# Kernel tuning notes

Measured on AMD Instinct MI355X. Metric: run time of the kernel, lower is better.

Reference implementation:

```python
import jax, jax.numpy as jnp
import numpy as np

B, N, D_IN, D = 4, 256, 128, 256
T = 3
EPS = 1e-5


def _layernorm(x, g, b):
    mu = x.mean(axis=-1, keepdims=True)
    var = x.var(axis=-1, keepdims=True)
    return (x - mu) * jax.lax.rsqrt(var + EPS) * g + b


def setup_inputs() -> dict:
    key = jax.random.key(0)
    ks = jax.random.split(key, 16)
    s = lambda k, shape, fan_in: jax.random.normal(k, shape, jnp.float32) / np.sqrt(fan_in)
    return {
        "inputs": jax.random.normal(ks[0], (B, N, D_IN), jnp.float32),
        "v_t": jax.random.normal(ks[1], (B, N, D), jnp.float32),
        "i_t": jnp.zeros((B, N, N), jnp.float32),
        # proj_inputs
        "Wp": s(ks[2], (D_IN, D), D_IN), "bp": jnp.zeros((D,), jnp.float32),
        # MLPAdjacency
        "Wx": s(ks[3], (D, D), D), "bx": jnp.zeros((D,), jnp.float32),
        "wi": s(ks[4], (D,), 1), "bi": jnp.zeros((D,), jnp.float32),
        "ws": s(ks[5], (D,), D), "bs": jnp.zeros((1,), jnp.float32),
        # LayerNorms
        "g_pre": jnp.ones((3 * D,), jnp.float32), "be_pre": jnp.zeros((3 * D,), jnp.float32),
        "g_n": jnp.ones((D,), jnp.float32), "be_n": jnp.zeros((D,), jnp.float32),
        # DeepSet(3D -> D -> D), equivariant layers: h@Wg + mean(h)@Wl + b
        "W1g": s(ks[6], (3 * D, D), 3 * D), "W1l": s(ks[7], (3 * D, D), 3 * D),
        "b1": jnp.zeros((D,), jnp.float32),
        "W2g": s(ks[8], (D, D), D), "W2l": s(ks[9], (D, D), D),
        "b2": jnp.zeros((D,), jnp.float32),
    }


def reference(inputs, v_t, i_t, Wp, bp, Wx, bx, wi, bi, ws, bs,
              g_pre, be_pre, g_n, be_n, W1g, W1l, b1, W2g, W2l, b2):
    x_in = inputs @ Wp + bp  # [b,n,d]
    n_t, inc = v_t, i_t
    preds = []
    for _ in range(T):
        # MLPAdjacency: [b,n,n,d] broadcast sum -> relu -> linear -> sigmoid
        xp = n_t @ Wx + bx
        s = jax.nn.relu(xp[:, None, :, :] + xp[:, :, None, :]
                        + inc[..., None] * wi + bi)
        inc = jax.nn.sigmoid(jnp.einsum('bend,d->ben', s, ws) + bs[0])  # [b,n,n]
        # aggregation
        upd = jnp.einsum('ben,bed->bnd', inc, n_t)
        # DeepSet over normalized concat, residual + LayerNorm
        h = _layernorm(jnp.concatenate([x_in, n_t, upd], axis=-1), g_pre, be_pre)
        m = h.mean(axis=1, keepdims=True)
        h1 = jax.nn.relu(h @ W1g + m @ W1l + b1)
        m1 = h1.mean(axis=1, keepdims=True)
        h2 = h1 @ W2g + m1 @ W2l + b2
        n_t = _layernorm(n_t + h2, g_n, be_n)
        preds.append(inc)
    return (jnp.stack(preds, axis=0), n_t, inc)
```

## Files before the change

kernel.cpp:

```cpp
#include <hip/hip_runtime.h>
#include <cstddef>

#define LN_EPS 1e-5f

__device__ inline float4 ld4(const float* p) { return *reinterpret_cast<const float4*>(p); }
__device__ inline void st4(float* p, float4 v) { *reinterpret_cast<float4*>(p) = v; }

__device__ __forceinline__ void gemm_dev(float* lds, const float* __restrict__ A,
                                         const float* __restrict__ W,
                                         const float* __restrict__ bias,
                                         float* __restrict__ dst,
                                         int K, int chunk, int row0, int col0, int k0) {
  float* At = lds;
  float* Ws = lds + 1088;
  const int tid = threadIdx.x;
  const int tx = tid & 15, ty = tid >> 4;
  float acc[4][4] = {{0.f}};
  const int arow = tid >> 2;
  const int ak4 = (tid & 3) * 4;
  const int wk = tid >> 4;
  const int wc4 = (tid & 15) * 4;
  for (int ks = 0; ks < chunk; ks += 16) {
    float4 av = ld4(&A[(size_t)(row0 + arow) * K + k0 + ks + ak4]);
    float4 wv = ld4(&W[(size_t)(k0 + ks + wk) * 256 + col0 + wc4]);
    __syncthreads();
    At[(ak4 + 0) * 68 + arow] = av.x;
    At[(ak4 + 1) * 68 + arow] = av.y;
    At[(ak4 + 2) * 68 + arow] = av.z;
    At[(ak4 + 3) * 68 + arow] = av.w;
    st4(&Ws[wk * 68 + wc4], wv);
    __syncthreads();
#pragma unroll
    for (int kk = 0; kk < 16; ++kk) {
      float4 a = ld4(&At[kk * 68 + ty * 4]);
      float4 w = ld4(&Ws[kk * 68 + tx * 4]);
      acc[0][0] = fmaf(a.x, w.x, acc[0][0]); acc[0][1] = fmaf(a.x, w.y, acc[0][1]);
      acc[0][2] = fmaf(a.x, w.z, acc[0][2]); acc[0][3] = fmaf(a.x, w.w, acc[0][3]);
      acc[1][0] = fmaf(a.y, w.x, acc[1][0]); acc[1][1] = fmaf(a.y, w.y, acc[1][1]);
      acc[1][2] = fmaf(a.y, w.z, acc[1][2]); acc[1][3] = fmaf(a.y, w.w, acc[1][3]);
      acc[2][0] = fmaf(a.z, w.x, acc[2][0]); acc[2][1] = fmaf(a.z, w.y, acc[2][1]);
      acc[2][2] = fmaf(a.z, w.z, acc[2][2]); acc[2][3] = fmaf(a.z, w.w, acc[2][3]);
      acc[3][0] = fmaf(a.w, w.x, acc[3][0]); acc[3][1] = fmaf(a.w, w.y, acc[3][1]);
      acc[3][2] = fmaf(a.w, w.z, acc[3][2]); acc[3][3] = fmaf(a.w, w.w, acc[3][3]);
    }
  }
  if (bias) {
    float4 b4 = ld4(&bias[col0 + tx * 4]);
#pragma unroll
    for (int i = 0; i < 4; ++i) {
      float4 o;
      o.x = acc[i][0] + b4.x; o.y = acc[i][1] + b4.y;
      o.z = acc[i][2] + b4.z; o.w = acc[i][3] + b4.w;
      st4(&dst[(size_t)(row0 + ty * 4 + i) * 256 + col0 + tx * 4], o);
    }
  } else {
#pragma unroll
    for (int i = 0; i < 4; ++i) {
      float4 o = {acc[i][0], acc[i][1], acc[i][2], acc[i][3]};
      st4(&dst[(size_t)(row0 + ty * 4 + i) * 256 + col0 + tx * 4], o);
    }
  }
}

__device__ __forceinline__ void gemm_h1(float* lds, const float* __restrict__ part,
                                        const float* __restrict__ mt1p,
                                        const float* __restrict__ W,
                                        float* __restrict__ dst,
                                        int gb, int row0, int col0, int k0) {
  float* At = lds;
  float* Ws = lds + 1088;
  float* mt1s = lds + 2176;
  const int tid = threadIdx.x;
  const int tx = tid & 15, ty = tid >> 4;
  if (tid < 64) {
    float s = 0.f;
#pragma unroll
    for (int k2 = 0; k2 < 12; ++k2) s += mt1p[((size_t)(k2 * 4 + gb) << 8) + k0 + tid];
    mt1s[tid] = s;
  }
  float acc[4][4] = {{0.f}};
  const int arow = tid >> 2;
  const int ak4 = (tid & 3) * 4;
  const int wk = tid >> 4;
  const int wc4 = (tid & 15) * 4;
  for (int ks = 0; ks < 64; ks += 16) {
    size_t ao = (size_t)(row0 + arow) * 256 + k0 + ks + ak4;
    float4 p0 = ld4(&part[ao]);
    float4 p1 = ld4(&part[ao + 262144]);
    float4 p2 = ld4(&part[ao + 524288]);
    float4 p3 = ld4(&part[ao + 786432]);
    float4 wv = ld4(&W[(size_t)(k0 + ks + wk) * 256 + col0 + wc4]);
    __syncthreads();
    float4 m = ld4(&mt1s[ks + ak4]);
    float4 av;
    av.x = fmaxf(p0.x + p1.x + p2.x + p3.x + m.x, 0.f);
    av.y = fmaxf(p0.y + p1.y + p2.y + p3.y + m.y, 0.f);
    av.z = fmaxf(p0.z + p1.z + p2.z + p3.z + m.z, 0.f);
    av.w = fmaxf(p0.w + p1.w + p2.w + p3.w + m.w, 0.f);
    At[(ak4 + 0) * 68 + arow] = av.x;
    At[(ak4 + 1) * 68 + arow] = av.y;
    At[(ak4 + 2) * 68 + arow] = av.z;
    At[(ak4 + 3) * 68 + arow] = av.w;
    st4(&Ws[wk * 68 + wc4], wv);
    __syncthreads();
#pragma unroll
    for (int kk = 0; kk < 16; ++kk) {
      float4 a = ld4(&At[kk * 68 + ty * 4]);
      float4 w = ld4(&Ws[kk * 68 + tx * 4]);
      acc[0][0] = fmaf(a.x, w.x, acc[0][0]); acc[0][1] = fmaf(a.x, w.y, acc[0][1]);
      acc[0][2] = fmaf(a.x, w.z, acc[0][2]); acc[0][3] = fmaf(a.x, w.w, acc[0][3]);
      acc[1][0] = fmaf(a.y, w.x, acc[1][0]); acc[1][1] = fmaf(a.y, w.y, acc[1][1]);
      acc[1][2] = fmaf(a.y, w.z, acc[1][2]); acc[1][3] = fmaf(a.y, w.w, acc[1][3]);
      acc[2][0] = fmaf(a.z, w.x, acc[2][0]); acc[2][1] = fmaf(a.z, w.y, acc[2][1]);
      acc[2][2] = fmaf(a.z, w.z, acc[2][2]); acc[2][3] = fmaf(a.z, w.w, acc[2][3]);
      acc[3][0] = fmaf(a.w, w.x, acc[3][0]); acc[3][1] = fmaf(a.w, w.y, acc[3][1]);
      acc[3][2] = fmaf(a.w, w.z, acc[3][2]); acc[3][3] = fmaf(a.w, w.w, acc[3][3]);
    }
  }
#pragma unroll
  for (int i = 0; i < 4; ++i) {
    float4 o = {acc[i][0], acc[i][1], acc[i][2], acc[i][3]};
    st4(&dst[(size_t)(row0 + ty * 4 + i) * 256 + col0 + tx * 4], o);
  }
}

__device__ __forceinline__ void gemmt_dev(float* lds, const float* __restrict__ pred,
                                          const float* __restrict__ nt,
                                          float* __restrict__ pp,
                                          int gb, int n0, int col0, int k0) {
  float* At = lds;
  float* Ws = lds + 1088;
  const int tid = threadIdx.x;
  const int tx = tid & 15, ty = tid >> 4;
  const float* Ab = pred + ((size_t)gb << 16);
  const float* Bb = nt + ((size_t)gb << 16);
  float acc[4][4] = {{0.f}};
  const int ee = tid >> 4;
  const int q4 = (tid & 15) * 4;
  for (int ks = 0; ks < 64; ks += 16) {
    float4 av = ld4(&Ab[((size_t)(k0 + ks + ee) << 8) + n0 + q4]);
    float4 wv = ld4(&Bb[((size_t)(k0 + ks + ee) << 8) + col0 + q4]);
    __syncthreads();
    st4(&At[ee * 68 + q4], av);
    st4(&Ws[ee * 68 + q4], wv);
    __syncthreads();
#pragma unroll
    for (int kk = 0; kk < 16; ++kk) {
      float4 a = ld4(&At[kk * 68 + ty * 4]);
      float4 w = ld4(&Ws[kk * 68 + tx * 4]);
      acc[0][0] = fmaf(a.x, w.x, acc[0][0]); acc[0][1] = fmaf(a.x, w.y, acc[0][1]);
      acc[0][2] = fmaf(a.x, w.z, acc[0][2]); acc[0][3] = fmaf(a.x, w.w, acc[0][3]);
      acc[1][0] = fmaf(a.y, w.x, acc[1][0]); acc[1][1] = fmaf(a.y, w.y, acc[1][1]);
      acc[1][2] = fmaf(a.y, w.z, acc[1][2]); acc[1][3] = fmaf(a.y, w.w, acc[1][3]);
      acc[2][0] = fmaf(a.z, w.x, acc[2][0]); acc[2][1] = fmaf(a.z, w.y, acc[2][1]);
      acc[2][2] = fmaf(a.z, w.z, acc[2][2]); acc[2][3] = fmaf(a.z, w.w, acc[2][3]);
      acc[3][0] = fmaf(a.w, w.x, acc[3][0]); acc[3][1] = fmaf(a.w, w.y, acc[3][1]);
      acc[3][2] = fmaf(a.w, w.z, acc[3][2]); acc[3][3] = fmaf(a.w, w.w, acc[3][3]);
    }
  }
#pragma unroll
  for (int i = 0; i < 4; ++i) {
    float4 o = {acc[i][0], acc[i][1], acc[i][2], acc[i][3]};
    st4(&pp[(((size_t)gb << 8) + n0 + ty * 4 + i) * 256 + col0 + tx * 4], o);
  }
}

__device__ __forceinline__ void wred2(float& s, float& q) {
#pragma unroll
  for (int off = 32; off; off >>= 1) {
    s += __shfl_xor(s, off);
    q += __shfl_xor(q, off);
  }
}

__device__ __forceinline__ void mtk_dev(float* lds, const float* __restrict__ X,
                                        const float* __restrict__ Wl,
                                        const float* __restrict__ bias,
                                        float* __restrict__ mtp, int gb, int ks, int Kd) {
  float* sm = lds;
  float* m64 = lds + 256;
  const int tid = threadIdx.x;
  const int col = tid & 63, q = tid >> 6;
  const float* xb = X + (size_t)(gb * 256 + q * 64) * Kd + ks * 64 + col;
  float s = 0.f;
#pragma unroll 8
  for (int r = 0; r < 64; ++r) s += xb[(size_t)r * Kd];
  sm[tid] = s;
  __syncthreads();
  if (tid < 64) m64[tid] = (sm[tid] + sm[tid + 64] + sm[tid + 128] + sm[tid + 192]) * (1.f / 256.f);
  __syncthreads();
  const int c = tid;
  float acc = (ks == 0) ? bias[c] : 0.f;
  const float* wp = Wl + (size_t)ks * 64 * 256 + c;
#pragma unroll 8
  for (int k = 0; k < 64; ++k) acc = fmaf(m64[k], wp[(size_t)k * 256], acc);
  mtp[((size_t)(ks * 4 + gb) << 8) + c] = acc;
}

__device__ __forceinline__ void mtk_h1(float* lds, const float* __restrict__ part,
                                       const float* __restrict__ mt1p,
                                       const float* __restrict__ Wl,
                                       const float* __restrict__ bias,
                                       float* __restrict__ mtp, int gb, int ks) {
  float* sm = lds;
  float* m64 = lds + 256;
  const int tid = threadIdx.x;
  const int col = tid & 63, q = tid >> 6;
  float mt1v = 0.f;
#pragma unroll
  for (int k2 = 0; k2 < 12; ++k2) mt1v += mt1p[((size_t)(k2 * 4 + gb) << 8) + ks * 64 + col];
  const float* pb = part + (size_t)(gb * 256 + q * 64) * 256 + ks * 64 + col;
  float s = 0.f;
#pragma unroll 4
  for (int r = 0; r < 64; ++r) {
    size_t o = (size_t)r * 256;
    float v = pb[o] + pb[o + 262144] + pb[o + 524288] + pb[o + 786432] + mt1v;
    s += fmaxf(v, 0.f);
  }
  sm[tid] = s;
  __syncthreads();
  if (tid < 64) m64[tid] = (sm[tid] + sm[tid + 64] + sm[tid + 128] + sm[tid + 192]) * (1.f / 256.f);
  __syncthreads();
  const int c = tid;
  float acc = (ks == 0) ? bias[c] : 0.f;
  const float* wp = Wl + (size_t)ks * 64 * 256 + c;
#pragma unroll 8
  for (int k = 0; k < 64; ++k) acc = fmaf(m64[k], wp[(size_t)k * 256], acc);
  mtp[((size_t)(ks * 4 + gb) << 8) + c] = acc;
}


__global__ __launch_bounds__(256) void k_gemm(const float* __restrict__ A,
                                              const float* __restrict__ W,
                                              const float* __restrict__ bias,
                                              float* __restrict__ dst,
                                              int K, int chunk) {
  __shared__ float lds[2176];
  float* base = bias ? dst : dst + (size_t)blockIdx.z * 262144;
  gemm_dev(lds, A, W, bias, base, K, chunk,
           blockIdx.x * 64, blockIdx.y * 64, blockIdx.z * chunk);
}

__global__ __launch_bounds__(256) void k_adj(const float* __restrict__ part,
                                             const float* __restrict__ incold,
                                             const float* __restrict__ wi,
                                             const float* __restrict__ bi,
                                             const float* __restrict__ bx,
                                             const float* __restrict__ wsv,
                                             const float* __restrict__ bs,
                                             float* __restrict__ pred,
                                             float* __restrict__ pred2) {
  __shared__ float lds[8448];
  float* tn = lds;
  float* te = lds + 32 * 132;
  const int n0 = blockIdx.x * 32, e0 = blockIdx.y * 32, gb = blockIdx.z;
  const int tid = threadIdx.x;
  const size_t rb = (size_t)gb * 256;
  const int tx = tid & 15, ty = tid >> 4;
  float incv[2][2], acc[2][2];
#pragma unroll
  for (int j = 0; j < 2; ++j)
#pragma unroll
    for (int i = 0; i < 2; ++i) {
      incv[j][i] = incold[((rb + e0 + ty + 16 * j) << 8) + n0 + tx + 16 * i];
      acc[j][i] = 0.f;
    }
  for (int dh = 0; dh < 256; dh += 128) {
    if (dh) __syncthreads();
#pragma unroll
    for (int s = 0; s < 4; ++s) {
      int idx = tid + s * 256;
      int row = idx >> 5;
      int d = dh + (idx & 31) * 4;
      float4 bxv = ld4(&bx[d]);
      {
        size_t o = ((rb + n0 + row) << 8) + d;
        float4 p0 = ld4(&part[o]);
        float4 p1 = ld4(&part[o + 262144]);
        float4 p2 = ld4(&part[o + 524288]);
        float4 p3 = ld4(&part[o + 786432]);
        float4 v;
        v.x = p0.x + p1.x + p2.x + p3.x + bxv.x;
        v.y = p0.y + p1.y + p2.y + p3.y + bxv.y;
        v.z = p0.z + p1.z + p2.z + p3.z + bxv.z;
        v.w = p0.w + p1.w + p2.w + p3.w + bxv.w;
        st4(&tn[row * 132 + (d - dh)], v);
      }
      {
        size_t o = ((rb + e0 + row) << 8) + d;
        float4 p0 = ld4(&part[o]);
        float4 p1 = ld4(&part[o + 262144]);
        float4 p2 = ld4(&part[o + 524288]);
        float4 p3 = ld4(&part[o + 786432]);
        float4 bv = ld4(&bi[d]);
        float4 v;
        v.x = p0.x + p1.x + p2.x + p3.x + bxv.x + bv.x;
        v.y = p0.y + p1.y + p2.y + p3.y + bxv.y + bv.y;
        v.z = p0.z + p1.z + p2.z + p3.z + bxv.z + bv.z;
        v.w = p0.w + p1.w + p2.w + p3.w + bxv.w + bv.w;
        st4(&te[row * 132 + (d - dh)], v);
      }
    }
    __syncthreads();
#pragma unroll 4
    for (int dl = 0; dl < 128; dl += 4) {
      float4 wiq = ld4(&wi[dh + dl]);
      float4 wsq = ld4(&wsv[dh + dl]);
      float4 xn0 = ld4(&tn[tx * 132 + dl]);
      float4 xn1 = ld4(&tn[(tx + 16) * 132 + dl]);
      float4 xe0 = ld4(&te[ty * 132 + dl]);
      float4 xe1 = ld4(&te[(ty + 16) * 132 + dl]);
#pragma unroll
      for (int j = 0; j < 2; ++j) {
        float4 xe = j ? xe1 : xe0;
#pragma unroll
        for (int i = 0; i < 2; ++i) {
          float4 xn = i ? xn1 : xn0;
          float u;
          u = fmaf(incv[j][i], wiq.x, xn.x + xe.x); u = fmaxf(u, 0.f); acc[j][i] = fmaf(u, wsq.x, acc[j][i]);
          u = fmaf(incv[j][i], wiq.y, xn.y + xe.y); u = fmaxf(u, 0.f); acc[j][i] = fmaf(u, wsq.y, acc[j][i]);
          u = fmaf(incv[j][i], wiq.z, xn.z + xe.z); u = fmaxf(u, 0.f); acc[j][i] = fmaf(u, wsq.z, acc[j][i]);
          u = fmaf(incv[j][i], wiq.w, xn.w + xe.w); u = fmaxf(u, 0.f); acc[j][i] = fmaf(u, wsq.w, acc[j][i]);
        }
      }
    }
  }
  const float b0 = bs[0];
#pragma unroll
  for (int j = 0; j < 2; ++j)
#pragma unroll
    for (int i = 0; i < 2; ++i) {
      float s = acc[j][i] + b0;
      float v = 1.f / (1.f + __expf(-s));
      size_t o = ((rb + e0 + ty + 16 * j) << 8) + n0 + tx + 16 * i;
      pred[o] = v;
      if (pred2) pred2[o] = v;
    }
}

__global__ __launch_bounds__(256) void k_gemmt(const float* __restrict__ pred,
                                               const float* __restrict__ nt,
                                               float* __restrict__ part) {
  __shared__ float lds[2176];
  const int gb = blockIdx.z >> 2, kc = blockIdx.z & 3;
  gemmt_dev(lds, pred, nt, part + (size_t)kc * 262144,
            gb, blockIdx.x * 64, blockIdx.y * 64, kc * 64);
}

__global__ __launch_bounds__(256) void k_ln768(const float* __restrict__ part,
                                               const float* __restrict__ x_in,
                                               const float* __restrict__ nt,
                                               const float* __restrict__ g,
                                               const float* __restrict__ be,
                                               float* __restrict__ h) {
  const int row = blockIdx.x * 4 + (threadIdx.x >> 6);
  const int lane = threadIdx.x & 63;
  const int c4 = lane * 4;
  const size_t ro = (size_t)row * 256 + c4;
  float4 u = ld4(&part[ro]);
  float4 u1 = ld4(&part[ro + 262144]);
  float4 u2 = ld4(&part[ro + 524288]);
  float4 u3 = ld4(&part[ro + 786432]);
  u.x += u1.x + u2.x + u3.x;
  u.y += u1.y + u2.y + u3.y;
  u.z += u1.z + u2.z + u3.z;
  u.w += u1.w + u2.w + u3.w;
  float4 xi = ld4(&x_in[ro]);
  float4 nv = ld4(&nt[ro]);
  float s = xi.x + xi.y + xi.z + xi.w + nv.x + nv.y + nv.z + nv.w + u.x + u.y + u.z + u.w;
  float sq = xi.x * xi.x + xi.y * xi.y + xi.z * xi.z + xi.w * xi.w
           + nv.x * nv.x + nv.y * nv.y + nv.z * nv.z + nv.w * nv.w
           + u.x * u.x + u.y * u.y + u.z * u.z + u.w * u.w;
  wred2(s, sq);
  float mu = s * (1.f / 768.f);
  float rs = rsqrtf(sq * (1.f / 768.f) - mu * mu + LN_EPS);
  float* hr = h + (size_t)row * 768;
  {
    float4 g4 = ld4(&g[c4]), b4 = ld4(&be[c4]), o;
    o.x = (xi.x - mu) * rs * g4.x + b4.x;
    o.y = (xi.y - mu) * rs * g4.y + b4.y;
    o.z = (xi.z - mu) * rs * g4.z + b4.z;
    o.w = (xi.w - mu) * rs * g4.w + b4.w;
    st4(&hr[c4], o);
  }
  {
    float4 g4 = ld4(&g[256 + c4]), b4 = ld4(&be[256 + c4]), o;
    o.x = (nv.x - mu) * rs * g4.x + b4.x;
    o.y = (nv.y - mu) * rs * g4.y + b4.y;
    o.z = (nv.z - mu) * rs * g4.z + b4.z;
    o.w = (nv.w - mu) * rs * g4.w + b4.w;
    st4(&hr[256 + c4], o);
  }
  {
    float4 g4 = ld4(&g[512 + c4]), b4 = ld4(&be[512 + c4]), o;
    o.x = (u.x - mu) * rs * g4.x + b4.x;
    o.y = (u.y - mu) * rs * g4.y + b4.y;
    o.z = (u.z - mu) * rs * g4.z + b4.z;
    o.w = (u.w - mu) * rs * g4.w + b4.w;
    st4(&hr[512 + c4], o);
  }
}

__global__ __launch_bounds__(256) void k_g768mtk(const float* __restrict__ h,
                                                 const float* __restrict__ W1g,
                                                 const float* __restrict__ W1l,
                                                 const float* __restrict__ b1,
                                                 float* __restrict__ part,
                                                 float* __restrict__ mt1p) {
  __shared__ float lds[2176];
  const int b = blockIdx.x;
  if (b < 256) {
    int mt = b & 15, ntile = (b >> 4) & 3, kz = b >> 6;
    gemm_dev(lds, h, W1g, nullptr, part + (size_t)kz * 262144, 768, 192,
             mt * 64, ntile * 64, kz * 192);
  } else {
    int idx = b - 256;
    mtk_dev(lds, h, W1l, b1, mt1p, idx & 3, idx >> 2, 768);
  }
}

__global__ __launch_bounds__(256) void k_gh1mtk2(const float* __restrict__ part,
                                                 const float* __restrict__ mt1p,
                                                 const float* __restrict__ W2g,
                                                 const float* __restrict__ W2l,
                                                 const float* __restrict__ b2,
                                                 float* __restrict__ part2,
                                                 float* __restrict__ mt2p) {
  __shared__ float lds[2240];
  const int b = blockIdx.x;
  if (b < 256) {
    int mt = b & 15, ntile = (b >> 4) & 3, kz = b >> 6;
    gemm_h1(lds, part, mt1p, W2g, part2 + (size_t)kz * 262144,
            mt >> 2, mt * 64, ntile * 64, kz * 64);
  } else {
    int idx = b - 256;
    mtk_h1(lds, part, mt1p, W2l, b2, mt2p, idx & 3, idx >> 2);
  }
}

__global__ __launch_bounds__(256) void k_ln256(const float* __restrict__ part2,
                                               const float* __restrict__ nt,
                                               const float* __restrict__ mt2p,
                                               const float* __restrict__ g,
                                               const float* __restrict__ be,
                                               float* __restrict__ dst) {
  const int row = blockIdx.x * 4 + (threadIdx.x >> 6);
  const int lane = threadIdx.x & 63;
  const int c4 = lane * 4;
  const int gb = row >> 8;
  const size_t ro = (size_t)row * 256 + c4;
  float4 p0 = ld4(&part2[ro]);
  float4 p1 = ld4(&part2[ro + 262144]);
  float4 p2 = ld4(&part2[ro + 524288]);
  float4 p3 = ld4(&part2[ro + 786432]);
  float4 m4 = {0.f, 0.f, 0.f, 0.f};
#pragma unroll
  for (int k2 = 0; k2 < 4; ++k2) {
    float4 mv = ld4(&mt2p[((size_t)(k2 * 4 + gb) << 8) + c4]);
    m4.x += mv.x; m4.y += mv.y; m4.z += mv.z; m4.w += mv.w;
  }
  float4 nv = ld4(&nt[ro]);
  float4 x;
  x.x = nv.x + p0.x + p1.x + p2.x + p3.x + m4.x;
  x.y = nv.y + p0.y + p1.y + p2.y + p3.y + m4.y;
  x.z = nv.z + p0.z + p1.z + p2.z + p3.z + m4.z;
  x.w = nv.w + p0.w + p1.w + p2.w + p3.w + m4.w;
  float s = x.x + x.y + x.z + x.w;
  float sq = x.x * x.x + x.y * x.y + x.z * x.z + x.w * x.w;
  wred2(s, sq);
  float mu = s * (1.f / 256.f);
  float rs = rsqrtf(sq * (1.f / 256.f) - mu * mu + LN_EPS);
  float4 g4 = ld4(&g[c4]), b4 = ld4(&be[c4]), o;
  o.x = (x.x - mu) * rs * g4.x + b4.x;
  o.y = (x.y - mu) * rs * g4.y + b4.y;
  o.z = (x.z - mu) * rs * g4.z + b4.z;
  o.w = (x.w - mu) * rs * g4.w + b4.w;
  st4(&dst[ro], o);
}

extern "C" void kernel_launch(void* const* d_in, const int* in_sizes, int n_in,
                              void* d_out, int out_size, void* d_ws, size_t ws_size,
                              hipStream_t stream) {
  (void)in_sizes; (void)n_in; (void)out_size; (void)ws_size;
  const float* inputs = (const float*)d_in[0];
  const float* v_t    = (const float*)d_in[1];
  const float* i_t    = (const float*)d_in[2];
  const float* Wp     = (const float*)d_in[3];
  const float* bp     = (const float*)d_in[4];
  const float* Wx     = (const float*)d_in[5];
  const float* bx     = (const float*)d_in[6];
  const float* wi     = (const float*)d_in[7];
  const float* bi     = (const float*)d_in[8];
  const float* ws     = (const float*)d_in[9];
  const float* bs     = (const float*)d_in[10];
  const float* g_pre  = (const float*)d_in[11];
  const float* be_pre = (const float*)d_in[12];
  const float* g_n    = (const float*)d_in[13];
  const float* be_n   = (const float*)d_in[14];
  const float* W1g    = (const float*)d_in[15];
  const float* W1l    = (const float*)d_in[16];
  const float* b1     = (const float*)d_in[17];
  const float* W2g    = (const float*)d_in[18];
  const float* W2l    = (const float*)d_in[19];
  const float* b2     = (const float*)d_in[20];
  float* out = (float*)d_out;
  float* wsf = (float*)d_ws;
  float* x_in  = wsf;
  float* ntA   = wsf + 262144;
  float* ntB   = wsf + 524288;
  float* h     = wsf + 786432;
  float* part2 = wsf + 786432;
  float* part  = wsf + 1835008;
  float* mt1p  = wsf + 2883584;
  float* mt2p  = wsf + 2895872;

  k_gemm<<<dim3(16, 4, 1), 256, 0, stream>>>(inputs, Wp, bp, x_in, 128, 128);

  for (int t = 0; t < 3; ++t) {
    const float* ntCur = (t == 0) ? v_t : ((t == 1) ? ntA : ntB);
    float* dstNt = (t == 2) ? (out + 786432) : ((t == 0) ? ntA : ntB);
    const float* incold = (t == 0) ? i_t : (out + (size_t)(t - 1) * 262144);
    float* pred = out + (size_t)t * 262144;
    float* pred2 = (t == 2) ? (out + 1048576) : nullptr;

    k_gemm<<<dim3(16, 4, 4), 256, 0, stream>>>(ntCur, Wx, nullptr, part, 256, 64);
    k_adj<<<dim3(8, 8, 4), 256, 0, stream>>>(part, incold, wi, bi, bx, ws, bs, pred, pred2);
    k_gemmt<<<dim3(4, 4, 16), 256, 0, stream>>>(pred, ntCur, part);
    k_ln768<<<256, 256, 0, stream>>>(part, x_in, ntCur, g_pre, be_pre, h);
    k_g768mtk<<<304, 256, 0, stream>>>(h, W1g, W1l, b1, part, mt1p);
    k_gh1mtk2<<<272, 256, 0, stream>>>(part, mt1p, W2g, W2l, b2, part2, mt2p);
    k_ln256<<<256, 256, 0, stream>>>(part2, ntCur, mt2p, g_n, be_n, dstNt);
  }
}
```

Measured before the change: 219.1 us.

## Prefetch next K-slice in GEMM loops and fuse input projection into first launch

Global loads for the next 16-wide K slice now go into registers after the LDS barrier, so they overlap the FMA loop of the current slice in gemm_dev, the relu-sum GEMM and gemmt. The input projection GEMM is merged with the first iteration's Wx GEMM into one 320-block launch, which removes a kernel launch and runs both workloads side by side. The prefetch adds register pressure, which may lower occupancy.

Result: faster. 198.6 us (-9.4%).

```diff
diff --git a/kernel.cpp b/kernel.cpp
--- a/kernel.cpp
+++ b/kernel.cpp
@@ -20,9 +20,9 @@
   const int ak4 = (tid & 3) * 4;
   const int wk = tid >> 4;
   const int wc4 = (tid & 15) * 4;
+  float4 av = ld4(&A[(size_t)(row0 + arow) * K + k0 + ak4]);
+  float4 wv = ld4(&W[(size_t)(k0 + wk) * 256 + col0 + wc4]);
   for (int ks = 0; ks < chunk; ks += 16) {
-    float4 av = ld4(&A[(size_t)(row0 + arow) * K + k0 + ks + ak4]);
-    float4 wv = ld4(&W[(size_t)(k0 + ks + wk) * 256 + col0 + wc4]);
     __syncthreads();
     At[(ak4 + 0) * 68 + arow] = av.x;
     At[(ak4 + 1) * 68 + arow] = av.y;
@@ -30,6 +30,10 @@
     At[(ak4 + 3) * 68 + arow] = av.w;
     st4(&Ws[wk * 68 + wc4], wv);
     __syncthreads();
+    if (ks + 16 < chunk) {
+      av = ld4(&A[(size_t)(row0 + arow) * K + k0 + ks + 16 + ak4]);
+      wv = ld4(&W[(size_t)(k0 + ks + 16 + wk) * 256 + col0 + wc4]);
+    }
 #pragma unroll
     for (int kk = 0; kk < 16; ++kk) {
       float4 a = ld4(&At[kk * 68 + ty * 4]);
@@ -83,13 +87,13 @@
   const int ak4 = (tid & 3) * 4;
   const int wk = tid >> 4;
   const int wc4 = (tid & 15) * 4;
+  size_t ao = (size_t)(row0 + arow) * 256 + k0 + ak4;
+  float4 p0 = ld4(&part[ao]);
+  float4 p1 = ld4(&part[ao + 262144]);
+  float4 p2 = ld4(&part[ao + 524288]);
+  float4 p3 = ld4(&part[ao + 786432]);
+  float4 wv = ld4(&W[(size_t)(k0 + wk) * 256 + col0 + wc4]);
   for (int ks = 0; ks < 64; ks += 16) {
-    size_t ao = (size_t)(row0 + arow) * 256 + k0 + ks + ak4;
-    float4 p0 = ld4(&part[ao]);
-    float4 p1 = ld4(&part[ao + 262144]);
-    float4 p2 = ld4(&part[ao + 524288]);
-    float4 p3 = ld4(&part[ao + 786432]);
-    float4 wv = ld4(&W[(size_t)(k0 + ks + wk) * 256 + col0 + wc4]);
     __syncthreads();
     float4 m = ld4(&mt1s[ks + ak4]);
     float4 av;
@@ -103,6 +107,14 @@
     At[(ak4 + 3) * 68 + arow] = av.w;
     st4(&Ws[wk * 68 + wc4], wv);
     __syncthreads();
+    if (ks + 16 < 64) {
+      size_t an = (size_t)(row0 + arow) * 256 + k0 + ks + 16 + ak4;
+      p0 = ld4(&part[an]);
+      p1 = ld4(&part[an + 262144]);
+      p2 = ld4(&part[an + 524288]);
+      p3 = ld4(&part[an + 786432]);
+      wv = ld4(&W[(size_t)(k0 + ks + 16 + wk) * 256 + col0 + wc4]);
+    }
 #pragma unroll
     for (int kk = 0; kk < 16; ++kk) {
       float4 a = ld4(&At[kk * 68 + ty * 4]);
@@ -137,13 +149,17 @@
   float acc[4][4] = {{0.f}};
   const int ee = tid >> 4;
   const int q4 = (tid & 15) * 4;
+  float4 av = ld4(&Ab[((size_t)(k0 + ee) << 8) + n0 + q4]);
+  float4 wv = ld4(&Bb[((size_t)(k0 + ee) << 8) + col0 + q4]);
   for (int ks = 0; ks < 64; ks += 16) {
-    float4 av = ld4(&Ab[((size_t)(k0 + ks + ee) << 8) + n0 + q4]);
-    float4 wv = ld4(&Bb[((size_t)(k0 + ks + ee) << 8) + col0 + q4]);
     __syncthreads();
     st4(&At[ee * 68 + q4], av);
     st4(&Ws[ee * 68 + q4], wv);
     __syncthreads();
+    if (ks + 16 < 64) {
+      av = ld4(&Ab[((size_t)(k0 + ks + 16 + ee) << 8) + n0 + q4]);
+      wv = ld4(&Bb[((size_t)(k0 + ks + 16 + ee) << 8) + col0 + q4]);
+    }
 #pragma unroll
     for (int kk = 0; kk < 16; ++kk) {
       float4 a = ld4(&At[kk * 68 + ty * 4]);
@@ -239,6 +255,26 @@
   float* base = bias ? dst : dst + (size_t)blockIdx.z * 262144;
   gemm_dev(lds, A, W, bias, base, K, chunk,
            blockIdx.x * 64, blockIdx.y * 64, blockIdx.z * chunk);
+}
+
+__global__ __launch_bounds__(256) void k_gemm0(const float* __restrict__ v_t,
+                                               const float* __restrict__ Wx,
+                                               float* __restrict__ part,
+                                               const float* __restrict__ inputs,
+                                               const float* __restrict__ Wp,
+                                               const float* __restrict__ bp,
+                                               float* __restrict__ x_in) {
+  __shared__ float lds[2176];
+  const int b = blockIdx.x;
+  if (b < 256) {
+    int mt = b & 15, ntile = (b >> 4) & 3, kz = b >> 6;
+    gemm_dev(lds, v_t, Wx, nullptr, part + (size_t)kz * 262144, 256, 64,
+             mt * 64, ntile * 64, kz * 64);
+  } else {
+    int idx = b - 256;
+    int mt = idx & 15, ntile = idx >> 4;
+    gemm_dev(lds, inputs, Wp, bp, x_in, 128, 128, mt * 64, ntile * 64, 0);
+  }
 }
 
 __global__ __launch_bounds__(256) void k_adj(const float* __restrict__ part,
@@ -514,8 +550,6 @@
   float* mt1p  = wsf + 2883584;
   float* mt2p  = wsf + 2895872;
 
-  k_gemm<<<dim3(16, 4, 1), 256, 0, stream>>>(inputs, Wp, bp, x_in, 128, 128);
-
   for (int t = 0; t < 3; ++t) {
     const float* ntCur = (t == 0) ? v_t : ((t == 1) ? ntA : ntB);
     float* dstNt = (t == 2) ? (out + 786432) : ((t == 0) ? ntA : ntB);
@@ -523,7 +557,11 @@
     float* pred = out + (size_t)t * 262144;
     float* pred2 = (t == 2) ? (out + 1048576) : nullptr;
 
-    k_gemm<<<dim3(16, 4, 4), 256, 0, stream>>>(ntCur, Wx, nullptr, part, 256, 64);
+    if (t == 0) {
+      k_gemm0<<<320, 256, 0, stream>>>(v_t, Wx, part, inputs, Wp, bp, x_in);
+    } else {
+      k_gemm<<<dim3(16, 4, 4), 256, 0, stream>>>(ntCur, Wx, nullptr, part, 256, 64);
+    }
     k_adj<<<dim3(8, 8, 4), 256, 0, stream>>>(part, incold, wi, bi, bx, ws, bs, pred, pred2);
     k_gemmt<<<dim3(4, 4, 16), 256, 0, stream>>>(pred, ntCur, part);
     k_ln768<<<256, 256, 0, stream>>>(part, x_in, ntCur, g_pre, be_pre, h);
```
